# Kernel tuning notes

Measured on AMD Instinct MI355X. Metric: run time of the kernel, lower is better.

Reference implementation:

```python
import jax, jax.numpy as jnp
import numpy as np
from jax import lax

QMAX = 15.0   # 4-bit unsigned activation levels
BN_EPS = 1e-5


def _binarize_irnet(w):
    # IR-Net style 1-bit weights: per-output-channel normalize, sign, rescale by mean |w|.
    mu = jnp.mean(w, axis=(1, 2, 3), keepdims=True)
    std = jnp.std(w, axis=(1, 2, 3), keepdims=True)
    wn = (w - mu) / (std + 1e-5)
    scale = jnp.mean(jnp.abs(wn), axis=(1, 2, 3), keepdims=True)
    wc = jnp.clip(wn, -1.0, 1.0)
    # STE: forward=sign(wn), backward=hardtanh passthrough
    bw = wc + lax.stop_gradient(jnp.sign(wn) - wc)
    return bw * scale


def _lsq_act_4bit(x, alpha):
    # LSQ unsigned 4-bit: clamp(x/alpha, 0, 15), round with STE, rescale.
    xs = jnp.clip(x / alpha, 0.0, QMAX)
    xq = xs + lax.stop_gradient(jnp.round(xs) - xs)
    return xq * alpha


def _qconv_bn_relu(x, w, alpha, g, b, m, v, stride):
    xq = _lsq_act_4bit(x, alpha)
    bw = _binarize_irnet(w)
    y = lax.conv_general_dilated(
        xq, bw, window_strides=(stride, stride), padding=((1, 1), (1, 1)),
        dimension_numbers=('NCHW', 'OIHW', 'NCHW'))
    inv = g / jnp.sqrt(v + BN_EPS)
    y = y * inv[None, :, None, None] + (b - m * inv)[None, :, None, None]
    return jax.nn.relu(y)


def setup_inputs() -> dict:
    key = jax.random.key(0)
    ks = jax.random.split(key, 3)
    B, C, H, W = 32, 256, 56, 56
    x = jax.random.normal(ks[0], (B, C, H, W), dtype=jnp.float32)
    w1 = jax.random.normal(ks[1], (C, C, 3, 3), dtype=jnp.float32) * 0.05
    w2 = jax.random.normal(ks[2], (C, C, 3, 3), dtype=jnp.float32) * 0.05
    ones = jnp.ones((C,), jnp.float32)
    zeros = jnp.zeros((C,), jnp.float32)
    return {
        'x': x,
        'w1': w1, 'alpha1': jnp.float32(0.1), 'g1': ones, 'b1': zeros, 'm1': zeros, 'v1': ones,
        'w2': w2, 'alpha2': jnp.float32(0.1), 'g2': ones, 'b2': zeros, 'm2': zeros, 'v2': ones,
    }


def reference(x, w1, alpha1, g1, b1, m1, v1, w2, alpha2, g2, b2, m2, v2):
    stride = 1
    h = _qconv_bn_relu(x, w1, alpha1, g1, b1, m1, v1, stride)
    out = _qconv_bn_relu(h, w2, alpha2, g2, b2, m2, v2, 1)
    return out
```

## Files before the change

kernel.cpp:

```cpp
#include <hip/hip_runtime.h>
#include <math.h>

typedef int v4i __attribute__((ext_vector_type(4)));
typedef int v16i __attribute__((ext_vector_type(16)));
typedef unsigned long long u64;

#define Bn 32
#define Cc 256
#define Hh 56
#define Ww 56
#define CSTR 136
#define RSTR (34 * CSTR)
#define ACT_LDS (9 * RSTR)

__device__ __forceinline__ float block_sum(float v, float* red) {
#pragma unroll
    for (int off = 32; off > 0; off >>= 1) v += __shfl_down(v, off, 64);
    const int wv = threadIdx.x >> 6;
    __syncthreads();
    if ((threadIdx.x & 63) == 0) red[wv] = v;
    __syncthreads();
    return red[0] + red[1] + red[2] + red[3];
}

__global__ __launch_bounds__(256) void k_binpack(const float* __restrict__ w,
                                                 signed char* __restrict__ wf,
                                                 float* __restrict__ wsc) {
    __shared__ float red[4];
    const int o = blockIdx.x;
    const float* wo = w + (size_t)o * 2304;
    const int t = threadIdx.x;
    float v[9];
    float s = 0.f, s2 = 0.f;
#pragma unroll
    for (int i = 0; i < 9; ++i) {
        v[i] = wo[t * 9 + i];
        s += v[i];
        s2 += v[i] * v[i];
    }
    s = block_sum(s, red);
    s2 = block_sum(s2, red);
    const float mu = s * (1.f / 2304.f);
    const float sd = sqrtf(fmaxf(s2 * (1.f / 2304.f) - mu * mu, 0.f));
    float sa = 0.f;
#pragma unroll
    for (int i = 0; i < 9; ++i) sa += fabsf(v[i] - mu);
    sa = block_sum(sa, red);
    if (t == 0) wsc[o] = (sa * (1.f / 2304.f)) / (sd + 1e-5f);
    const int c = t, c32 = c >> 5, hf = (c >> 4) & 1, j = c & 15;
    const int lane = (hf << 5) | (o & 31), octile = o >> 5;
#pragma unroll
    for (int tap = 0; tap < 9; ++tap) {
        const float d = v[tap] - mu;
        const signed char sg = (d > 0.f) ? 1 : ((d < 0.f) ? -1 : 0);
        wf[(size_t)(((tap * 8 + c32) * 8 + octile) * 64 + lane) * 16 + j] = sg;
    }
}

__global__ void k_prep(const float* __restrict__ g1, const float* __restrict__ b1,
                       const float* __restrict__ m1, const float* __restrict__ v1,
                       const float* __restrict__ g2, const float* __restrict__ b2,
                       const float* __restrict__ m2, const float* __restrict__ v2,
                       const float* __restrict__ a1p, const float* __restrict__ a2p,
                       const float* __restrict__ ws1, const float* __restrict__ ws2,
                       float* __restrict__ ep) {
    const int i = threadIdx.x;
    const float i1 = g1[i] / sqrtf(v1[i] + 1e-5f);
    const float i2 = g2[i] / sqrtf(v2[i] + 1e-5f);
    ep[i] = a1p[0] * ws1[i] * i1;
    ep[256 + i] = b1[i] - m1[i] * i1;
    ep[512 + i] = a2p[0] * ws2[i] * i2;
    ep[768 + i] = b2[i] - m2[i] * i2;
}

__global__ __launch_bounds__(256) void k_quant_nhwc(const float* __restrict__ x,
                                                    unsigned char* __restrict__ xq,
                                                    const float* __restrict__ ap) {
    __shared__ unsigned char q[3584];
    const int bid = blockIdx.x;
    const int cg = bid & 3;
    const int h = (bid >> 2) % Hh;
    const int n = bid / (4 * Hh);
    const float a = ap[0];
    const int c0 = cg * 64;
    for (int i = threadIdx.x; i < 3584; i += 256) {
        const int cl = i / 56;
        const int w = i - cl * 56;
        const float v = x[(((size_t)n * Cc + c0 + cl) * Hh + h) * Ww + w];
        const float xs = fminf(fmaxf(v / a, 0.f), 15.f);
        q[w * 64 + (((cl >> 2) ^ (w & 15)) << 2) + (cl & 3)] = (unsigned char)(int)rintf(xs);
    }
    __syncthreads();
    const unsigned int* q32 = (const unsigned int*)q;
    unsigned int* dst = (unsigned int*)xq + ((size_t)(n * Hh + h) * Ww) * 32;
    for (int j = threadIdx.x; j < 448; j += 256) {
        const int w = j >> 3, g8l = (j >> 1) & 3, hf = j & 1;
        const unsigned int lo = q32[w * 16 + ((g8l * 4 + hf) ^ (w & 15))];
        const unsigned int hi = q32[w * 16 + ((g8l * 4 + 2 + hf) ^ (w & 15))];
        dst[w * 32 + (cg * 4 + g8l) * 2 + hf] = lo | (hi << 4);
    }
}

__device__ __forceinline__ v4i unp(u64 p) {
    const unsigned int lo = (unsigned int)p, hi = (unsigned int)(p >> 32);
    v4i b;
    b[0] = (int)(lo & 0x0F0F0F0Fu);
    b[1] = (int)(hi & 0x0F0F0F0Fu);
    b[2] = (int)((lo >> 4) & 0x0F0F0F0Fu);
    b[3] = (int)((hi >> 4) & 0x0F0F0F0Fu);
    return b;
}

template <bool QOUT>
__global__ __launch_bounds__(256, 2) void k_conv(const unsigned char* __restrict__ xin,
                                                 const signed char* __restrict__ wf,
                                                 const float* __restrict__ ep,
                                                 const float* __restrict__ a2p,
                                                 unsigned char* __restrict__ hq,
                                                 float* __restrict__ yout) {
    __shared__ __align__(16) unsigned char sm[ACT_LDS];
    const int bid = blockIdx.x;
    const int oh = bid & 1;
    const int mh = (bid >> 1) & 1;
    const int hb = (bid >> 2) & 7;
    const int n = bid >> 5;
    const int h0 = hb * 7;
    const int mbase = mh * 32;
    const int tid = threadIdx.x;

    for (int u = tid; u < 9 * 34 * 16; u += 256) {
        const int r = u / 544;
        const int rem = u - r * 544;
        const int col = rem >> 4;
        const int t8 = rem & 15;
        const int y = h0 - 1 + r;
        const int xi = mbase - 1 + col;
        u64 v = 0;
        if ((unsigned)y < 56u && (unsigned)xi < 56u)
            v = *(const u64*)(xin + ((((size_t)n * Hh + y) * Ww + xi) << 7) + (t8 << 3));
        *(u64*)(sm + r * RSTR + col * CSTR + (t8 << 3)) = v;
    }
    __syncthreads();

    const int lane = tid & 63;
    const int g = tid >> 6;
    const int half = lane >> 5;
    const int lm = lane & 31;
    const int octile = oh * 4 + g;

    v16i acc[7] = {};
    const v4i* wpg = (const v4i*)wf + octile * 64 + lane;
    const unsigned char* bp0 = sm + lm * CSTR + half * 8;

#pragma unroll 1
    for (int c32 = 0; c32 < 8; ++c32) {
        v4i aw[9];
#pragma unroll
        for (int tap = 0; tap < 9; ++tap) aw[tap] = wpg[(tap * 8 + c32) << 9];
        const unsigned char* bp = bp0 + c32 * 16;
#pragma unroll
        for (int kw = 0; kw < 3; ++kw) {
            v4i bfr[9];
#pragma unroll
            for (int ar = 0; ar < 9; ++ar)
                bfr[ar] = unp(*(const u64*)(bp + kw * CSTR + ar * RSTR));
#pragma unroll
            for (int kh = 0; kh < 3; ++kh) {
#pragma unroll
                for (int r = 0; r < 7; ++r)
                    acc[r] = __builtin_amdgcn_mfma_i32_32x32x32_i8(aw[kh * 3 + kw],
                                                                   bfr[r + kh], acc[r], 0, 0, 0);
            }
        }
    }

    if constexpr (QOUT) {
        __syncthreads();
        unsigned int* hb = (unsigned int*)sm;
        const float inva = 1.0f / a2p[0];
        const int oc0w = oh * 128 + g * 32;
        const int d0 = 4 * g + half;
#pragma unroll
        for (int r = 0; r < 7; ++r) {
            const v16i av = acc[r];
            unsigned int pk0 = 0, pk1 = 0;
#pragma unroll
            for (int q = 0; q < 4; ++q) {
                const int oc = oc0w + 4 * half + q;
                const unsigned int c0 = (unsigned int)(int)rintf(
                    fminf(fmaxf(fmaf((float)av[q], ep[oc], ep[256 + oc]), 0.f) * inva, 15.f));
                const unsigned int c1 = (unsigned int)(int)rintf(
                    fminf(fmaxf(fmaf((float)av[4 + q], ep[oc + 8], ep[264 + oc]), 0.f) * inva, 15.f));
                const unsigned int c2 = (unsigned int)(int)rintf(
                    fminf(fmaxf(fmaf((float)av[8 + q], ep[oc + 16], ep[272 + oc]), 0.f) * inva, 15.f));
                const unsigned int c3 = (unsigned int)(int)rintf(
                    fminf(fmaxf(fmaf((float)av[12 + q], ep[oc + 24], ep[280 + oc]), 0.f) * inva, 15.f));
                pk0 |= (c0 | (c1 << 4)) << (8 * q);
                pk1 |= (c2 | (c3 << 4)) << (8 * q);
            }
            const int rb = (r * 32 + lm) * 16;
            hb[rb + (d0 ^ (lm & 15))] = pk0;
            hb[rb + ((d0 + 2) ^ (lm & 15))] = pk1;
        }
        __syncthreads();
        unsigned int* dst = (unsigned int*)hq;
        for (int j = tid; j < 7 * 32 * 16; j += 256) {
            const int rw = j >> 4, dw = j & 15;
            const int r = rw >> 5, wl = rw & 31;
            const int w = mbase + wl;
            if (w < 56)
                dst[((size_t)((n * Hh + h0 + r) * Ww) + w) * 32 + oh * 16 + dw] =
                    hb[(rw << 4) + (dw ^ (wl & 15))];
        }
    } else {
        const int w = mbase + lm;
        if (w < 56) {
            float* dst = yout + (size_t)n * Cc * 3136 + (size_t)h0 * 56 + w;
#pragma unroll
            for (int r = 0; r < 7; ++r) {
                const v16i av = acc[r];
#pragma unroll
                for (int reg = 0; reg < 16; ++reg) {
                    const int oc = oh * 128 + g * 32 + (reg & 3) + 8 * (reg >> 2) + 4 * half;
                    dst[(size_t)oc * 3136 + r * 56] =
                        fmaxf(fmaf((float)av[reg], ep[oc], ep[256 + oc]), 0.f);
                }
            }
        }
    }
}

extern "C" void kernel_launch(void* const* d_in, const int* in_sizes, int n_in,
                              void* d_out, int out_size, void* d_ws, size_t ws_size,
                              hipStream_t stream) {
    const float* x = (const float*)d_in[0];
    const float* w1 = (const float*)d_in[1];
    const float* a1 = (const float*)d_in[2];
    const float* g1 = (const float*)d_in[3];
    const float* b1 = (const float*)d_in[4];
    const float* m1 = (const float*)d_in[5];
    const float* v1 = (const float*)d_in[6];
    const float* w2 = (const float*)d_in[7];
    const float* a2 = (const float*)d_in[8];
    const float* g2 = (const float*)d_in[9];
    const float* b2 = (const float*)d_in[10];
    const float* m2 = (const float*)d_in[11];
    const float* v2 = (const float*)d_in[12];

    signed char* wf1 = (signed char*)d_ws;
    signed char* wf2 = wf1 + 589824;
    float* wsc1 = (float*)(wf2 + 589824);
    float* wsc2 = wsc1 + 256;
    float* ep = wsc2 + 256;
    unsigned char* xq1 = (unsigned char*)(ep + 1024);
    unsigned char* hq = xq1 + (size_t)12845056;

    k_binpack<<<256, 256, 0, stream>>>(w1, wf1, wsc1);
    k_binpack<<<256, 256, 0, stream>>>(w2, wf2, wsc2);
    k_prep<<<1, 256, 0, stream>>>(g1, b1, m1, v1, g2, b2, m2, v2, a1, a2, wsc1, wsc2, ep);
    k_quant_nhwc<<<Bn * Hh * 4, 256, 0, stream>>>(x, xq1, a1);

    k_conv<true><<<1024, 256, 0, stream>>>(xq1, wf1, ep, a2, hq, nullptr);
    k_conv<false><<<1024, 256, 0, stream>>>(hq, wf2, ep + 512, nullptr, nullptr, (float*)d_out);
}
```

Measured before the change: 208.8 us.

## Read zero-padded byte-per-code NHWC activations directly from global memory in conv

Activations move from a packed 4-bit NHWC layout staged through LDS to an unpacked one-byte-per-code NHWC layout with a zero border. The conv kernel now loads its MFMA B fragments straight from global memory, which removes the LDS staging, the bounds checks and the nibble unpacking. Each block covers 4 output rows instead of 7, giving 1792 blocks and allowing 3 blocks per CU. In exchange the activation tensors double in size, rows overlapping between blocks are re-read from global or cache, and an extra kernel is added to zero the border of the intermediate buffer.

```diff
diff --git a/kernel.cpp b/kernel.cpp
--- a/kernel.cpp
+++ b/kernel.cpp
@@ -9,9 +9,9 @@
 #define Cc 256
 #define Hh 56
 #define Ww 56
-#define CSTR 136
-#define RSTR (34 * CSTR)
-#define ACT_LDS (9 * RSTR)
+#define PD 58
+#define PROW (PD * 256)
+#define PIMG ((size_t)PD * PROW)
 
 __device__ __forceinline__ float block_sum(float v, float* red) {
 #pragma unroll
@@ -73,151 +73,140 @@
     ep[768 + i] = b2[i] - m2[i] * i2;
 }
 
-__global__ __launch_bounds__(256) void k_quant_nhwc(const float* __restrict__ x,
-                                                    unsigned char* __restrict__ xq,
-                                                    const float* __restrict__ ap) {
-    __shared__ unsigned char q[3584];
-    const int bid = blockIdx.x;
-    const int cg = bid & 3;
-    const int h = (bid >> 2) % Hh;
-    const int n = bid / (4 * Hh);
+__global__ __launch_bounds__(256) void k_quant_pad(const float* __restrict__ x,
+                                                   unsigned char* __restrict__ xp,
+                                                   const float* __restrict__ ap) {
+    const int yp = blockIdx.x % PD;
+    const int n = blockIdx.x / PD;
+    unsigned char* row = xp + (size_t)n * PIMG + (size_t)yp * PROW;
+    if (yp == 0 || yp == PD - 1) {
+        const v4i z = {0, 0, 0, 0};
+        for (int j = threadIdx.x; j < PROW / 16; j += 256) ((v4i*)row)[j] = z;
+        return;
+    }
     const float a = ap[0];
-    const int c0 = cg * 64;
-    for (int i = threadIdx.x; i < 3584; i += 256) {
-        const int cl = i / 56;
-        const int w = i - cl * 56;
-        const float v = x[(((size_t)n * Cc + c0 + cl) * Hh + h) * Ww + w];
-        const float xs = fminf(fmaxf(v / a, 0.f), 15.f);
-        q[w * 64 + (((cl >> 2) ^ (w & 15)) << 2) + (cl & 3)] = (unsigned char)(int)rintf(xs);
-    }
-    __syncthreads();
-    const unsigned int* q32 = (const unsigned int*)q;
-    unsigned int* dst = (unsigned int*)xq + ((size_t)(n * Hh + h) * Ww) * 32;
-    for (int j = threadIdx.x; j < 448; j += 256) {
-        const int w = j >> 3, g8l = (j >> 1) & 3, hf = j & 1;
-        const unsigned int lo = q32[w * 16 + ((g8l * 4 + hf) ^ (w & 15))];
-        const unsigned int hi = q32[w * 16 + ((g8l * 4 + 2 + hf) ^ (w & 15))];
-        dst[w * 32 + (cg * 4 + g8l) * 2 + hf] = lo | (hi << 4);
-    }
-}
-
-__device__ __forceinline__ v4i unp(u64 p) {
-    const unsigned int lo = (unsigned int)p, hi = (unsigned int)(p >> 32);
-    v4i b;
-    b[0] = (int)(lo & 0x0F0F0F0Fu);
-    b[1] = (int)(hi & 0x0F0F0F0Fu);
-    b[2] = (int)((lo >> 4) & 0x0F0F0F0Fu);
-    b[3] = (int)((hi >> 4) & 0x0F0F0F0Fu);
-    return b;
+    const int c = threadIdx.x;
+    const int h = yp - 1;
+    const float* src = x + ((size_t)(n * Cc + c) * Hh + h) * Ww;
+    unsigned char codes[56];
+#pragma unroll
+    for (int w4 = 0; w4 < 14; ++w4) {
+        const float4 v = ((const float4*)src)[w4];
+        codes[w4 * 4 + 0] = (unsigned char)(int)rintf(fminf(fmaxf(v.x / a, 0.f), 15.f));
+        codes[w4 * 4 + 1] = (unsigned char)(int)rintf(fminf(fmaxf(v.y / a, 0.f), 15.f));
+        codes[w4 * 4 + 2] = (unsigned char)(int)rintf(fminf(fmaxf(v.z / a, 0.f), 15.f));
+        codes[w4 * 4 + 3] = (unsigned char)(int)rintf(fminf(fmaxf(v.w / a, 0.f), 15.f));
+    }
+    row[c] = 0;
+    row[57 * 256 + c] = 0;
+#pragma unroll
+    for (int w = 0; w < 56; ++w) row[(w + 1) * 256 + c] = codes[w];
+}
+
+__global__ __launch_bounds__(256) void k_zero_border(unsigned char* __restrict__ hp) {
+    const int n = blockIdx.x;
+    unsigned char* img = hp + (size_t)n * PIMG;
+    const v4i z = {0, 0, 0, 0};
+    for (int j = threadIdx.x; j < 2 * PROW / 16; j += 256) {
+        const int yp = (j < PROW / 16) ? 0 : (PD - 1);
+        const int jj = (j < PROW / 16) ? j : j - PROW / 16;
+        ((v4i*)(img + (size_t)yp * PROW))[jj] = z;
+    }
+    for (int j = threadIdx.x; j < 56 * 2 * 16; j += 256) {
+        const int y = 1 + (j >> 5);
+        const int xcol = ((j >> 4) & 1) * (PD - 1);
+        const int q = j & 15;
+        ((v4i*)(img + (size_t)y * PROW + xcol * 256))[q] = z;
+    }
 }
 
 template <bool QOUT>
-__global__ __launch_bounds__(256, 2) void k_conv(const unsigned char* __restrict__ xin,
+__global__ __launch_bounds__(256, 3) void k_conv(const unsigned char* __restrict__ xpad,
                                                  const signed char* __restrict__ wf,
                                                  const float* __restrict__ ep,
                                                  const float* __restrict__ a2p,
-                                                 unsigned char* __restrict__ hq,
+                                                 unsigned char* __restrict__ hpad,
                                                  float* __restrict__ yout) {
-    __shared__ __align__(16) unsigned char sm[ACT_LDS];
+    __shared__ unsigned int hb[4 * 32 * 32];
     const int bid = blockIdx.x;
     const int oh = bid & 1;
     const int mh = (bid >> 1) & 1;
-    const int hb = (bid >> 2) & 7;
-    const int n = bid >> 5;
-    const int h0 = hb * 7;
+    const int hblk = (bid >> 2) % 14;
+    const int n = (bid >> 2) / 14;
+    const int h0 = hblk * 4;
     const int mbase = mh * 32;
     const int tid = threadIdx.x;
-
-    for (int u = tid; u < 9 * 34 * 16; u += 256) {
-        const int r = u / 544;
-        const int rem = u - r * 544;
-        const int col = rem >> 4;
-        const int t8 = rem & 15;
-        const int y = h0 - 1 + r;
-        const int xi = mbase - 1 + col;
-        u64 v = 0;
-        if ((unsigned)y < 56u && (unsigned)xi < 56u)
-            v = *(const u64*)(xin + ((((size_t)n * Hh + y) * Ww + xi) << 7) + (t8 << 3));
-        *(u64*)(sm + r * RSTR + col * CSTR + (t8 << 3)) = v;
-    }
-    __syncthreads();
-
     const int lane = tid & 63;
     const int g = tid >> 6;
     const int half = lane >> 5;
     const int lm = lane & 31;
     const int octile = oh * 4 + g;
 
-    v16i acc[7] = {};
+    v16i acc[4] = {};
     const v4i* wpg = (const v4i*)wf + octile * 64 + lane;
-    const unsigned char* bp0 = sm + lm * CSTR + half * 8;
+    const unsigned char* bbase = xpad + (size_t)n * PIMG + (size_t)h0 * PROW +
+                                 (mbase + lm) * 256 + half * 16;
 
 #pragma unroll 1
     for (int c32 = 0; c32 < 8; ++c32) {
         v4i aw[9];
 #pragma unroll
         for (int tap = 0; tap < 9; ++tap) aw[tap] = wpg[(tap * 8 + c32) << 9];
-        const unsigned char* bp = bp0 + c32 * 16;
+        const unsigned char* bc = bbase + (c32 << 5);
 #pragma unroll
         for (int kw = 0; kw < 3; ++kw) {
-            v4i bfr[9];
-#pragma unroll
-            for (int ar = 0; ar < 9; ++ar)
-                bfr[ar] = unp(*(const u64*)(bp + kw * CSTR + ar * RSTR));
-#pragma unroll
-            for (int kh = 0; kh < 3; ++kh) {
-#pragma unroll
-                for (int r = 0; r < 7; ++r)
+            v4i bfr[6];
+#pragma unroll
+            for (int rr = 0; rr < 6; ++rr)
+                bfr[rr] = *(const v4i*)(bc + kw * 256 + rr * PROW);
+#pragma unroll
+            for (int kh = 0; kh < 3; ++kh)
+#pragma unroll
+                for (int r = 0; r < 4; ++r)
                     acc[r] = __builtin_amdgcn_mfma_i32_32x32x32_i8(aw[kh * 3 + kw],
                                                                    bfr[r + kh], acc[r], 0, 0, 0);
+        }
+    }
+
+    if constexpr (QOUT) {
+        const float inva = 1.0f / a2p[0];
+        const int ocb = oh * 128 + g * 32;
+#pragma unroll
+        for (int r = 0; r < 4; ++r) {
+            const v16i av = acc[r];
+#pragma unroll
+            for (int hi4 = 0; hi4 < 4; ++hi4) {
+                unsigned int pk = 0;
+#pragma unroll
+                for (int q = 0; q < 4; ++q) {
+                    const int oc = ocb + 4 * half + 8 * hi4 + q;
+                    const unsigned int cq = (unsigned int)(int)rintf(
+                        fminf(fmaxf(fmaf((float)av[hi4 * 4 + q], ep[oc], ep[256 + oc]), 0.f) * inva,
+                              15.f));
+                    pk |= cq << (8 * q);
+                }
+                const int d = g * 8 + half + 2 * hi4;
+                hb[(r * 32 + lm) * 32 + (d ^ lm)] = pk;
             }
         }
-    }
-
-    if constexpr (QOUT) {
         __syncthreads();
-        unsigned int* hb = (unsigned int*)sm;
-        const float inva = 1.0f / a2p[0];
-        const int oc0w = oh * 128 + g * 32;
-        const int d0 = 4 * g + half;
-#pragma unroll
-        for (int r = 0; r < 7; ++r) {
-            const v16i av = acc[r];
-            unsigned int pk0 = 0, pk1 = 0;
-#pragma unroll
-            for (int q = 0; q < 4; ++q) {
-                const int oc = oc0w + 4 * half + q;
-                const unsigned int c0 = (unsigned int)(int)rintf(
-                    fminf(fmaxf(fmaf((float)av[q], ep[oc], ep[256 + oc]), 0.f) * inva, 15.f));
-                const unsigned int c1 = (unsigned int)(int)rintf(
-                    fminf(fmaxf(fmaf((float)av[4 + q], ep[oc + 8], ep[264 + oc]), 0.f) * inva, 15.f));
-                const unsigned int c2 = (unsigned int)(int)rintf(
-                    fminf(fmaxf(fmaf((float)av[8 + q], ep[oc + 16], ep[272 + oc]), 0.f) * inva, 15.f));
-                const unsigned int c3 = (unsigned int)(int)rintf(
-                    fminf(fmaxf(fmaf((float)av[12 + q], ep[oc + 24], ep[280 + oc]), 0.f) * inva, 15.f));
-                pk0 |= (c0 | (c1 << 4)) << (8 * q);
-                pk1 |= (c2 | (c3 << 4)) << (8 * q);
+        for (int j = tid; j < 4096; j += 256) {
+            const int dw = j & 31;
+            const int xx = (j >> 5) & 31;
+            const int r = j >> 10;
+            if (mbase + xx < 56) {
+                unsigned int* dst = (unsigned int*)(hpad + (size_t)n * PIMG +
+                                                    (size_t)(h0 + 1 + r) * PROW +
+                                                    (mbase + 1 + xx) * 256 + oh * 128);
+                dst[dw] = hb[(r * 32 + xx) * 32 + (dw ^ xx)];
             }
-            const int rb = (r * 32 + lm) * 16;
-            hb[rb + (d0 ^ (lm & 15))] = pk0;
-            hb[rb + ((d0 + 2) ^ (lm & 15))] = pk1;
-        }
-        __syncthreads();
-        unsigned int* dst = (unsigned int*)hq;
-        for (int j = tid; j < 7 * 32 * 16; j += 256) {
-            const int rw = j >> 4, dw = j & 15;
-            const int r = rw >> 5, wl = rw & 31;
-            const int w = mbase + wl;
-            if (w < 56)
-                dst[((size_t)((n * Hh + h0 + r) * Ww) + w) * 32 + oh * 16 + dw] =
-                    hb[(rw << 4) + (dw ^ (wl & 15))];
         }
     } else {
         const int w = mbase + lm;
         if (w < 56) {
             float* dst = yout + (size_t)n * Cc * 3136 + (size_t)h0 * 56 + w;
 #pragma unroll
-            for (int r = 0; r < 7; ++r) {
+            for (int r = 0; r < 4; ++r) {
                 const v16i av = acc[r];
 #pragma unroll
                 for (int reg = 0; reg < 16; ++reg) {
@@ -252,14 +241,15 @@
     float* wsc1 = (float*)(wf2 + 589824);
     float* wsc2 = wsc1 + 256;
     float* ep = wsc2 + 256;
-    unsigned char* xq1 = (unsigned char*)(ep + 1024);
-    unsigned char* hq = xq1 + (size_t)12845056;
+    unsigned char* xpad = (unsigned char*)(ep + 1024);
+    unsigned char* hpad = xpad + PIMG * Bn + 4096;
 
     k_binpack<<<256, 256, 0, stream>>>(w1, wf1, wsc1);
     k_binpack<<<256, 256, 0, stream>>>(w2, wf2, wsc2);
     k_prep<<<1, 256, 0, stream>>>(g1, b1, m1, v1, g2, b2, m2, v2, a1, a2, wsc1, wsc2, ep);
-    k_quant_nhwc<<<Bn * Hh * 4, 256, 0, stream>>>(x, xq1, a1);
-
-    k_conv<true><<<1024, 256, 0, stream>>>(xq1, wf1, ep, a2, hq, nullptr);
-    k_conv<false><<<1024, 256, 0, stream>>>(hq, wf2, ep + 512, nullptr, nullptr, (float*)d_out);
-}
+    k_quant_pad<<<Bn * PD, 256, 0, stream>>>(x, xpad, a1);
+    k_zero_border<<<Bn, 256, 0, stream>>>(hpad);
+
+    k_conv<true><<<1792, 256, 0, stream>>>(xpad, wf1, ep, a2, hpad, nullptr);
+    k_conv<false><<<1792, 256, 0, stream>>>(hpad, wf2, ep + 512, nullptr, nullptr, (float*)d_out);
+}
```

Result: slower. 344.2 us (+64.9%).
